# Kernel optimization log

Hardware: AMD Instinct MI355X
Metric: run time of the kernel (lower is better)

## Reference

```python
import jax, jax.numpy as jnp
import numpy as np

N_SURF, N_GRAPH, K_EIG = 30000, 12000, 128
C_IN_SURF, C_IN_GRAPH, C_OUT = 5, 20, 1
HID = 64  # C_width // 2
N_BLOCK = 4
NEIGH_TH = 8.0
BOX = 90.0
E_GRAPH = 192000


def _build_bipartite(rng):
    # exact math of compute_bipartite_graphs: cdist < neigh_th, w = exp(-d/sigma)
    verts = rng.random((N_SURF, 3), dtype=np.float32) * BOX
    pos = rng.random((N_GRAPH, 3), dtype=np.float32) * BOX
    sigma = NEIGH_TH / 2.0
    srcs, dsts, ws = [], [], []
    pn = (pos * pos).sum(-1)
    for s in range(0, N_SURF, 2048):
        ch = verts[s:s + 2048]
        d2 = (ch * ch).sum(-1)[:, None] + pn[None, :] - 2.0 * ch @ pos.T
        d = np.sqrt(np.maximum(d2, 0.0))
        ii, jj = np.where(d < NEIGH_TH)
        srcs.append(ii + s)
        dsts.append(jj + N_SURF)  # graph nodes offset by n_surf
        ws.append(np.exp(-d[ii, jj] / sigma))
    return (np.concatenate(srcs).astype(np.int64),
            np.concatenate(dsts).astype(np.int64),
            np.concatenate(ws).astype(np.float32))


def setup_inputs() -> dict:
    key = jax.random.key(0)
    ks = iter(jax.random.split(key, 64))
    rng = np.random.default_rng(0)
    bi_surf, bi_graph, bi_w = _build_bipartite(rng)

    def rn(shape, scale=0.05):
        return jax.random.normal(next(ks), shape, jnp.float32) * scale

    inp = {
        'x_surf': rn((N_SURF, C_IN_SURF), 1.0),
        'x_graph': rn((N_GRAPH, C_IN_GRAPH), 1.0),
        'mass': jax.random.uniform(next(ks), (N_SURF,), jnp.float32) + 0.1,
        'evals': jnp.sort(jax.random.uniform(next(ks), (K_EIG,), jnp.float32)) * 100.0,
        'evecs': rn((N_SURF, K_EIG), 1.0) / np.sqrt(N_SURF),
        'bi_w': jnp.asarray(bi_w),
        'lin1_w': rn((C_IN_SURF, HID)), 'lin1_b': jnp.zeros((HID,), jnp.float32),
        'lin2_w': rn((C_IN_GRAPH, HID)), 'lin2_b': jnp.zeros((HID,), jnp.float32),
        'diff_time': jax.random.uniform(next(ks), (N_BLOCK, HID), jnp.float32) * 0.1 + 1e-3,
        'mlp_w0': rn((N_BLOCK, 2 * HID, HID)), 'mlp_b0': jnp.zeros((N_BLOCK, HID), jnp.float32),
        'mlp_w1': rn((N_BLOCK, HID, HID)), 'mlp_b1': jnp.zeros((N_BLOCK, HID), jnp.float32),
        'mlp_w2': rn((N_BLOCK, HID, HID)), 'mlp_b2': jnp.zeros((N_BLOCK, HID), jnp.float32),
        'gcn_w1': rn((N_BLOCK, HID, HID)), 'gcn_b1': jnp.zeros((N_BLOCK, HID), jnp.float32),
        'gcn_w2': rn((N_BLOCK, HID, HID)), 'gcn_b2': jnp.zeros((N_BLOCK, HID), jnp.float32),
        'gs_w': rn((N_BLOCK - 1, HID, HID)), 'gs_b': jnp.zeros((N_BLOCK - 1, HID), jnp.float32),
        'gs_w_last': rn((HID, C_OUT)), 'gs_b_last': jnp.zeros((C_OUT,), jnp.float32),
        'sg_w': rn((N_BLOCK - 1, HID, HID)), 'sg_b': jnp.zeros((N_BLOCK - 1, HID), jnp.float32),
        'sg_w_last': rn((HID, C_OUT)), 'sg_b_last': jnp.zeros((C_OUT,), jnp.float32),
        'graph_edge_index': jax.random.randint(next(ks), (2, E_GRAPH), 0, N_GRAPH, jnp.int64),
        'bi_surf': jnp.asarray(bi_surf),
        'bi_graph': jnp.asarray(bi_graph),
    }
    return inp


def gcn_conv(x, W, b, src, dst, ew, n):
    # PyG GCNConv: sym-normalized aggregation with self loops (weight 1)
    h = x @ W
    w = ew if ew is not None else jnp.ones(src.shape, x.dtype)
    deg = jnp.ones((n,), x.dtype).at[dst].add(w)
    dinv = jnp.where(deg > 0, jax.lax.rsqrt(deg), 0.0)
    norm = dinv[src] * dinv[dst] * w
    out = jnp.zeros((n, h.shape[1]), x.dtype).at[dst].add(norm[:, None] * h[src])
    return out + (dinv * dinv)[:, None] * h + b


def reference(x_surf, x_graph, mass, evals, evecs, bi_w,
              lin1_w, lin1_b, lin2_w, lin2_b,
              diff_time, mlp_w0, mlp_b0, mlp_w1, mlp_b1, mlp_w2, mlp_b2,
              gcn_w1, gcn_b1, gcn_w2, gcn_b2,
              gs_w, gs_b, gs_w_last, gs_b_last,
              sg_w, sg_b, sg_w_last, sg_b_last,
              graph_edge_index, bi_surf, bi_graph):
    n_surf, n_graph = x_surf.shape[0], x_graph.shape[0]
    n_tot = n_surf + n_graph
    diff_x = x_surf @ lin1_w + lin1_b            # [Ns, HID]
    g_x = x_graph @ lin2_w + lin2_b              # [Ng, HID]
    gsrc, gdst = graph_edge_index[0], graph_edge_index[1]

    for i in range(N_BLOCK):
        # --- DiffusionNet block (spectral diffusion + MLP + skip) ---
        t = jnp.clip(diff_time[i], 1e-8)
        x_spec = evecs.T @ (mass[:, None] * diff_x)                  # [K, HID]
        x_diffuse = evecs @ (jnp.exp(-evals[:, None] * t[None, :]) * x_spec)
        feat = jnp.concatenate([diff_x, x_diffuse], axis=-1)
        h = jax.nn.relu(feat @ mlp_w0[i] + mlp_b0[i])
        h = jax.nn.relu(h @ mlp_w1[i] + mlp_b1[i])
        h = h @ mlp_w2[i] + mlp_b2[i]
        diff_x = diff_x + h
        # --- internal GCN on molecular graph (use_distance=False) ---
        hg = jax.nn.relu(gcn_conv(g_x, gcn_w1[i], gcn_b1[i], gsrc, gdst, None, n_graph))
        g_x = gcn_conv(hg, gcn_w2[i], gcn_b2[i], gsrc, gdst, None, n_graph)
        # --- bipartite mixing over combined node set ---
        x_cat = jnp.concatenate([diff_x, g_x], axis=0)               # [Ns+Ng, HID]
        if i < N_BLOCK - 1:
            new_surf = gcn_conv(x_cat, gs_w[i], gs_b[i], bi_graph, bi_surf, bi_w, n_tot)[:n_surf]
            new_graph = gcn_conv(x_cat, sg_w[i], sg_b[i], bi_surf, bi_graph, bi_w, n_tot)[n_surf:]
        else:
            new_surf = gcn_conv(x_cat, gs_w_last, gs_b_last, bi_graph, bi_surf, bi_w, n_tot)[:n_surf]
            new_graph = gcn_conv(x_cat, sg_w_last, sg_b_last, bi_surf, bi_graph, bi_w, n_tot)[n_surf:]
        diff_x, g_x = new_surf, new_graph

    return jnp.concatenate([diff_x, g_x], axis=0)  # [Ns+Ng, C_out]
```

## Files before the change

### kernel.cpp

```cpp
#include <hip/hip_runtime.h>

#define N_SURF 30000
#define N_GRAPH 12000
#define K_EIG 128
#define HID 64
#define E_GRAPH 192000
#define NPART 240

static inline int cdiv(int a, int b) { return (a + b - 1) / b; }

__global__ void k_fill(float* __restrict__ p, float v, int n) {
    int t = blockIdx.x * blockDim.x + threadIdx.x;
    if (t < n) p[t] = v;
}

__global__ void k_filli(int* __restrict__ p, int v, int n) {
    int t = blockIdx.x * blockDim.x + threadIdx.x;
    if (t < n) p[t] = v;
}

__global__ void k_to_dinv(float* __restrict__ p, int n) {
    int t = blockIdx.x * blockDim.x + threadIdx.x;
    if (t < n) p[t] = 1.0f / sqrtf(p[t]);
}

__global__ void k_deg_hist_bi(const int* __restrict__ bs, const int* __restrict__ bg,
                              const float* __restrict__ w, float* __restrict__ deg_s,
                              float* __restrict__ deg_g, int* __restrict__ cnt_s,
                              int* __restrict__ cnt_g, int E) {
    int t = blockIdx.x * blockDim.x + threadIdx.x;
    if (t < E) {
        int s = bs[t], g = bg[t] - N_SURF;
        float wv = w[t];
        atomicAdd(&deg_s[s], wv);
        atomicAdd(&deg_g[g], wv);
        atomicAdd(&cnt_s[s], 1);
        atomicAdd(&cnt_g[g], 1);
    }
}

__global__ void k_deg_hist_gr(const int* __restrict__ gdst, float* __restrict__ deg,
                              int* __restrict__ cnt, int E) {
    int t = blockIdx.x * blockDim.x + threadIdx.x;
    if (t < E) {
        int d = gdst[t];
        atomicAdd(&deg[d], 1.0f);
        atomicAdd(&cnt[d], 1);
    }
}

__global__ __launch_bounds__(256) void k_scan(const int* __restrict__ cnt,
                                              int* __restrict__ rowptr, int n) {
    __shared__ int part[256];
    int per = (n + 255) / 256;
    int lo = threadIdx.x * per, hi = min(lo + per, n);
    int s = 0;
    for (int i = lo; i < hi; ++i) s += cnt[i];
    part[threadIdx.x] = s;
    __syncthreads();
    for (int off = 1; off < 256; off <<= 1) {
        int v = (threadIdx.x >= off) ? part[threadIdx.x - off] : 0;
        __syncthreads();
        part[threadIdx.x] += v;
        __syncthreads();
    }
    int base = (threadIdx.x == 0) ? 0 : part[threadIdx.x - 1];
    for (int i = lo; i < hi; ++i) { rowptr[i] = base; base += cnt[i]; }
    if (threadIdx.x == 0) rowptr[n] = part[255];
}

__global__ void k_fill_csr_s_seq(const int* __restrict__ bs, const int* __restrict__ bg,
                                 const float* __restrict__ w, const float* __restrict__ dinv_s,
                                 int2* __restrict__ csr, int E) {
    int t = blockIdx.x * blockDim.x + threadIdx.x;
    if (t >= E) return;
    int s = bs[t], g = bg[t] - N_SURF;
    csr[t] = make_int2(g, __float_as_int(dinv_s[s] * w[t]));
}

__global__ void k_fill_csr_g(const int* __restrict__ bs, const int* __restrict__ bg,
                             const float* __restrict__ w, const float* __restrict__ dinv_g,
                             const int* __restrict__ rp, int* __restrict__ cur,
                             int2* __restrict__ csr, int E) {
    int t = blockIdx.x * blockDim.x + threadIdx.x;
    if (t >= E) return;
    int s = bs[t], g = bg[t] - N_SURF;
    int pp = rp[g] + atomicAdd(&cur[g], 1);
    csr[pp] = make_int2(s, __float_as_int(dinv_g[g] * w[t]));
}

__global__ void k_fill_csr_gr(const int* __restrict__ ei, const float* __restrict__ dinv,
                              const int* __restrict__ rp, int* __restrict__ cur,
                              int2* __restrict__ csr, int E) {
    int t = blockIdx.x * blockDim.x + threadIdx.x;
    if (t >= E) return;
    int s = ei[t], d = ei[E + t];
    int pp = rp[d] + atomicAdd(&cur[d], 1);
    csr[pp] = make_int2(s, __float_as_int(dinv[s] * dinv[d]));
}

__global__ void k_lin(const float* __restrict__ X, const float* __restrict__ W,
                      const float* __restrict__ b, float* __restrict__ out, int M, int K) {
    int t = blockIdx.x * blockDim.x + threadIdx.x;
    if (t >= M * HID) return;
    int r = t >> 6, h = t & 63;
    float acc = b[h];
    for (int k = 0; k < K; ++k) acc = fmaf(X[r * K + k], W[k * HID + h], acc);
    out[t] = acc;
}

__global__ __launch_bounds__(256) void k_spec_part(const float* __restrict__ evecs,
                                                   const float* __restrict__ mass,
                                                   const float* __restrict__ dx,
                                                   float* __restrict__ partial) {
    __shared__ float evs[32 * 128];
    __shared__ float xms[32 * 64];
    const int h = threadIdx.x & 63, eg = threadIdx.x >> 6;
    float acc[32];
#pragma unroll
    for (int i = 0; i < 32; ++i) acc[i] = 0.f;
    for (int r0 = blockIdx.x * 32; r0 < N_SURF; r0 += gridDim.x * 32) {
        __syncthreads();
        for (int idx = threadIdx.x; idx < 32 * 128; idx += 256) {
            int rr = idx >> 7, k = idx & 127;
            int row = r0 + rr;
            evs[idx] = (row < N_SURF) ? evecs[(size_t)row * 128 + k] : 0.f;
        }
        for (int idx = threadIdx.x; idx < 32 * 64; idx += 256) {
            int rr = idx >> 6, c = idx & 63;
            int row = r0 + rr;
            xms[idx] = (row < N_SURF) ? mass[row] * dx[(size_t)row * 64 + c] : 0.f;
        }
        __syncthreads();
        for (int rr = 0; rr < 32; ++rr) {
            float xv = xms[rr * 64 + h];
            const float* ep = &evs[rr * 128 + eg * 32];
#pragma unroll
            for (int e = 0; e < 32; ++e) acc[e] = fmaf(ep[e], xv, acc[e]);
        }
    }
    float* outp = &partial[(size_t)blockIdx.x * 8192];
#pragma unroll
    for (int e = 0; e < 32; ++e) outp[(eg * 32 + e) * 64 + h] = acc[e];
}

__global__ void k_spec_reduce_bscale(const float* __restrict__ partial,
                                     const float* __restrict__ evals,
                                     const float* __restrict__ t,
                                     float* __restrict__ Bsc) {
    int idx = blockIdx.x * blockDim.x + threadIdx.x;
    if (idx >= 128 * 64) return;
    int k = idx >> 6, h = idx & 63;
    float s = 0.f;
    for (int b = 0; b < NPART; ++b) s += partial[(size_t)b * 8192 + idx];
    float tt = fmaxf(t[h], 1e-8f);
    Bsc[idx] = expf(-evals[k] * tt) * s;
}

template <int K, bool RELU_A>
__global__ __launch_bounds__(256) void k_gemm64(const float* __restrict__ A1,
                                                const float* __restrict__ A2, int M1,
                                                const float* __restrict__ B,
                                                float* __restrict__ C, int M) {
    __shared__ float Bs[K * 64];
    __shared__ float As[64 * K];
    for (int idx = threadIdx.x; idx < K * 64; idx += 256) Bs[idx] = B[idx];
    const int h = threadIdx.x & 63, rg = threadIdx.x >> 6;
    for (int r0 = blockIdx.x * 64; r0 < M; r0 += gridDim.x * 64) {
        __syncthreads();
        for (int idx = threadIdx.x; idx < 64 * K; idx += 256) {
            int rr = idx / K, k = idx - rr * K;
            int row = r0 + rr;
            float v = 0.f;
            if (row < M) {
                v = (row < M1) ? A1[(size_t)row * K + k]
                               : A2[(size_t)(row - M1) * K + k];
                if (RELU_A) v = fmaxf(v, 0.f);
            }
            As[idx] = v;
        }
        __syncthreads();
        float acc[16];
#pragma unroll
        for (int i = 0; i < 16; ++i) acc[i] = 0.f;
        for (int k = 0; k < K; k += 4) {
            float b0 = Bs[(k + 0) * 64 + h], b1 = Bs[(k + 1) * 64 + h];
            float b2 = Bs[(k + 2) * 64 + h], b3 = Bs[(k + 3) * 64 + h];
#pragma unroll
            for (int i = 0; i < 16; ++i) {
                const float* ap = &As[(rg * 16 + i) * K + k];
                acc[i] = fmaf(ap[0], b0, fmaf(ap[1], b1, fmaf(ap[2], b2, fmaf(ap[3], b3, acc[i]))));
            }
        }
#pragma unroll
        for (int i = 0; i < 16; ++i) {
            int row = r0 + rg * 16 + i;
            if (row < M) C[(size_t)row * 64 + h] = acc[i];
        }
    }
}

__global__ __launch_bounds__(256) void k_gemm128_r32(const float* __restrict__ A,
                                                     const float* __restrict__ B,
                                                     float* __restrict__ C, int M) {
    __shared__ float Bs[128 * 64];
    __shared__ float As[32 * 128];
    for (int idx = threadIdx.x; idx < 128 * 64; idx += 256) Bs[idx] = B[idx];
    const int h = threadIdx.x & 63, rg = threadIdx.x >> 6;
    for (int r0 = blockIdx.x * 32; r0 < M; r0 += gridDim.x * 32) {
        __syncthreads();
        for (int idx = threadIdx.x; idx < 32 * 128; idx += 256) {
            int rr = idx >> 7, k = idx & 127;
            int row = r0 + rr;
            As[idx] = (row < M) ? A[(size_t)row * 128 + k] : 0.f;
        }
        __syncthreads();
        float acc[8];
#pragma unroll
        for (int i = 0; i < 8; ++i) acc[i] = 0.f;
        for (int k = 0; k < 128; k += 4) {
            float b0 = Bs[(k + 0) * 64 + h], b1 = Bs[(k + 1) * 64 + h];
            float b2 = Bs[(k + 2) * 64 + h], b3 = Bs[(k + 3) * 64 + h];
#pragma unroll
            for (int i = 0; i < 8; ++i) {
                const float* ap = &As[(rg * 8 + i) * 128 + k];
                acc[i] = fmaf(ap[0], b0, fmaf(ap[1], b1, fmaf(ap[2], b2, fmaf(ap[3], b3, acc[i]))));
            }
        }
#pragma unroll
        for (int i = 0; i < 8; ++i) {
            int row = r0 + rg * 8 + i;
            if (row < M) C[(size_t)row * 64 + h] = acc[i];
        }
    }
}

__global__ __launch_bounds__(256) void k_mlp(float* __restrict__ dx, const float* __restrict__ xd,
                                             const float* __restrict__ w0, const float* __restrict__ b0,
                                             const float* __restrict__ w1, const float* __restrict__ b1,
                                             const float* __restrict__ w2, const float* __restrict__ b2,
                                             int M) {
    __shared__ float w0s[128 * 64];
    __shared__ float w1s[64 * 64];
    __shared__ float w2s[64 * 64];
    __shared__ float bsh[3][64];
    __shared__ float feat[4][128];
    __shared__ float h1s[4][64];
    __shared__ float h2s[4][64];
    for (int idx = threadIdx.x; idx < 8192; idx += 256) w0s[idx] = w0[idx];
    for (int idx = threadIdx.x; idx < 4096; idx += 256) { w1s[idx] = w1[idx]; w2s[idx] = w2[idx]; }
    if (threadIdx.x < 64) {
        bsh[0][threadIdx.x] = b0[threadIdx.x];
        bsh[1][threadIdx.x] = b1[threadIdx.x];
        bsh[2][threadIdx.x] = b2[threadIdx.x];
    }
    const int h = threadIdx.x & 63, rg = threadIdx.x >> 6;
    for (int r0 = blockIdx.x * 4; r0 < M; r0 += gridDim.x * 4) {
        int r = r0 + rg;
        __syncthreads();
        feat[rg][h] = dx[(size_t)r * 64 + h];
        feat[rg][64 + h] = xd[(size_t)r * 64 + h];
        __syncthreads();
        float acc = bsh[0][h];
        for (int k = 0; k < 128; k += 4) {
            const float* fp = &feat[rg][k];
            acc = fmaf(fp[0], w0s[(k + 0) * 64 + h],
                  fmaf(fp[1], w0s[(k + 1) * 64 + h],
                  fmaf(fp[2], w0s[(k + 2) * 64 + h],
                  fmaf(fp[3], w0s[(k + 3) * 64 + h], acc))));
        }
        h1s[rg][h] = fmaxf(acc, 0.f);
        __syncthreads();
        acc = bsh[1][h];
        for (int k = 0; k < 64; k += 4) {
            const float* fp = &h1s[rg][k];
            acc = fmaf(fp[0], w1s[(k + 0) * 64 + h],
                  fmaf(fp[1], w1s[(k + 1) * 64 + h],
                  fmaf(fp[2], w1s[(k + 2) * 64 + h],
                  fmaf(fp[3], w1s[(k + 3) * 64 + h], acc))));
        }
        h2s[rg][h] = fmaxf(acc, 0.f);
        __syncthreads();
        acc = bsh[2][h];
        for (int k = 0; k < 64; k += 4) {
            const float* fp = &h2s[rg][k];
            acc = fmaf(fp[0], w2s[(k + 0) * 64 + h],
                  fmaf(fp[1], w2s[(k + 1) * 64 + h],
                  fmaf(fp[2], w2s[(k + 2) * 64 + h],
                  fmaf(fp[3], w2s[(k + 3) * 64 + h], acc))));
        }
        dx[(size_t)r * 64 + h] += acc;
    }
}

__global__ __launch_bounds__(256) void k_gather64(
    const int* __restrict__ rowptr, const int2* __restrict__ csr,
    const float* __restrict__ Hsrc, const float* __restrict__ Hself,
    const float* __restrict__ dinv, const float* __restrict__ b,
    float* __restrict__ out, int M) {
    int r = blockIdx.x * 4 + (threadIdx.x >> 6);
    int h = threadIdx.x & 63;
    if (r >= M) return;
    int e0 = rowptr[r], e1 = rowptr[r + 1];
    float dv = dinv[r];
    float acc = fmaf(dv * dv, Hself[(size_t)r * 64 + h], b[h]);
    int e = e0;
    for (; e + 1 < e1; e += 2) {
        int2 c0 = csr[e], c1 = csr[e + 1];
        acc = fmaf(__int_as_float(c0.y), Hsrc[(size_t)c0.x * 64 + h], acc);
        acc = fmaf(__int_as_float(c1.y), Hsrc[(size_t)c1.x * 64 + h], acc);
    }
    if (e < e1) {
        int2 c = csr[e];
        acc = fmaf(__int_as_float(c.y), Hsrc[(size_t)c.x * 64 + h], acc);
    }
    out[(size_t)r * 64 + h] = acc;
}

__global__ __launch_bounds__(256) void k_gather1(
    const int* __restrict__ rowptr, const int2* __restrict__ csr,
    const float* __restrict__ H1src, const float* __restrict__ H1self,
    const float* __restrict__ dinv, const float* __restrict__ b,
    float* __restrict__ out, int M) {
    int r = blockIdx.x * 4 + (threadIdx.x >> 6);
    int l = threadIdx.x & 63;
    if (r >= M) return;
    int e0 = rowptr[r], e1 = rowptr[r + 1];
    float acc = 0.f;
    for (int e = e0 + l; e < e1; e += 64) {
        int2 c = csr[e];
        acc = fmaf(__int_as_float(c.y), H1src[c.x], acc);
    }
    for (int off = 32; off; off >>= 1) acc += __shfl_down(acc, off, 64);
    if (l == 0) {
        float dv = dinv[r];
        out[r] = fmaf(dv * dv, H1self[r], b[0]) + acc;
    }
}

__global__ void k_gemv64c(const float* __restrict__ A1, const float* __restrict__ A2, int M1,
                          const float* __restrict__ w, float* __restrict__ out, int M) {
    int gid = blockIdx.x * blockDim.x + threadIdx.x;
    int r = gid >> 6, l = gid & 63;
    if (r >= M) return;
    const float* row = (r < M1) ? &A1[(size_t)r * 64] : &A2[(size_t)(r - M1) * 64];
    float v = row[l] * w[l];
    for (int off = 32; off; off >>= 1) v += __shfl_down(v, off, 64);
    if (l == 0) out[r] = v;
}

extern "C" void kernel_launch(void* const* d_in, const int* in_sizes, int n_in,
                              void* d_out, int out_size, void* d_ws, size_t ws_size,
                              hipStream_t stream) {
    const float* x_surf   = (const float*)d_in[0];
    const float* x_graph  = (const float*)d_in[1];
    const float* mass     = (const float*)d_in[2];
    const float* evals    = (const float*)d_in[3];
    const float* evecs    = (const float*)d_in[4];
    const float* bi_w     = (const float*)d_in[5];
    const float* lin1_w   = (const float*)d_in[6];
    const float* lin1_b   = (const float*)d_in[7];
    const float* lin2_w   = (const float*)d_in[8];
    const float* lin2_b   = (const float*)d_in[9];
    const float* diff_time= (const float*)d_in[10];
    const float* mlp_w0   = (const float*)d_in[11];
    const float* mlp_b0   = (const float*)d_in[12];
    const float* mlp_w1   = (const float*)d_in[13];
    const float* mlp_b1   = (const float*)d_in[14];
    const float* mlp_w2   = (const float*)d_in[15];
    const float* mlp_b2   = (const float*)d_in[16];
    const float* gcn_w1   = (const float*)d_in[17];
    const float* gcn_b1   = (const float*)d_in[18];
    const float* gcn_w2   = (const float*)d_in[19];
    const float* gcn_b2   = (const float*)d_in[20];
    const float* gs_w     = (const float*)d_in[21];
    const float* gs_b     = (const float*)d_in[22];
    const float* gs_w_last= (const float*)d_in[23];
    const float* gs_b_last= (const float*)d_in[24];
    const float* sg_w     = (const float*)d_in[25];
    const float* sg_b     = (const float*)d_in[26];
    const float* sg_w_last= (const float*)d_in[27];
    const float* sg_b_last= (const float*)d_in[28];
    const int* graph_ei   = (const int*)d_in[29];
    const int* bi_s       = (const int*)d_in[30];
    const int* bi_g       = (const int*)d_in[31];
    const int E = in_sizes[5];
    float* out = (float*)d_out;

    float* p = (float*)d_ws;
    float* surfA = p; p += (size_t)N_SURF * 64;
    float* surfB = p; p += (size_t)N_SURF * 64;
    float* xd    = p; p += (size_t)N_SURF * 64;
    float* hcat  = p; p += (size_t)(N_SURF + N_GRAPH) * 64;
    float* gA    = p; p += (size_t)N_GRAPH * 64;
    float* gB    = p; p += (size_t)N_GRAPH * 64;
    float* tmpg  = p; p += (size_t)N_GRAPH * 64;
    float* hg    = p; p += (size_t)N_GRAPH * 64;
    float* partial = p; p += (size_t)NPART * 8192;
    float* Bsc   = p; p += 128 * 64;
    float* dinv_s  = p; p += N_SURF;
    float* dinv_g  = p; p += N_GRAPH;
    float* dinv_gr = p; p += N_GRAPH;
    int* cnt_s = (int*)p; p += N_SURF;
    int* cnt_g = (int*)p; p += N_GRAPH;
    int* cnt_gr= (int*)p; p += N_GRAPH;
    int* rp_s  = (int*)p; p += N_SURF + 1;
    int* rp_g  = (int*)p; p += N_GRAPH + 1;
    int* rp_gr = (int*)p; p += N_GRAPH + 1;
    p += ((size_t)p & 4) ? 1 : 0;
    int2* csr_s  = (int2*)p; p += 2 * (size_t)E;
    int2* csr_g  = (int2*)p; p += 2 * (size_t)E;
    int2* csr_gr = (int2*)p; p += 2 * (size_t)E_GRAPH;

    float* hg_part = hcat + (size_t)N_SURF * 64;
    float* dx  = surfA;
    float* nsx = surfB;
    float* gx  = gA;
    float* gx2 = gB;

    k_lin<<<cdiv(N_SURF * 64, 256), 256, 0, stream>>>(x_surf, lin1_w, lin1_b, dx, N_SURF, 5);
    k_lin<<<cdiv(N_GRAPH * 64, 256), 256, 0, stream>>>(x_graph, lin2_w, lin2_b, gx, N_GRAPH, 20);
    k_fill<<<cdiv(N_SURF, 256), 256, 0, stream>>>(dinv_s, 1.f, N_SURF);
    k_fill<<<cdiv(N_GRAPH, 256), 256, 0, stream>>>(dinv_g, 1.f, N_GRAPH);
    k_fill<<<cdiv(N_GRAPH, 256), 256, 0, stream>>>(dinv_gr, 1.f, N_GRAPH);
    k_filli<<<cdiv(N_SURF, 256), 256, 0, stream>>>(cnt_s, 0, N_SURF);
    k_filli<<<cdiv(N_GRAPH, 256), 256, 0, stream>>>(cnt_g, 0, N_GRAPH);
    k_filli<<<cdiv(N_GRAPH, 256), 256, 0, stream>>>(cnt_gr, 0, N_GRAPH);
    k_deg_hist_bi<<<cdiv(E, 256), 256, 0, stream>>>(bi_s, bi_g, bi_w, dinv_s, dinv_g,
                                                    cnt_s, cnt_g, E);
    k_deg_hist_gr<<<cdiv(E_GRAPH, 256), 256, 0, stream>>>(graph_ei + E_GRAPH, dinv_gr, cnt_gr, E_GRAPH);
    k_to_dinv<<<cdiv(N_SURF, 256), 256, 0, stream>>>(dinv_s, N_SURF);
    k_to_dinv<<<cdiv(N_GRAPH, 256), 256, 0, stream>>>(dinv_g, N_GRAPH);
    k_to_dinv<<<cdiv(N_GRAPH, 256), 256, 0, stream>>>(dinv_gr, N_GRAPH);
    k_scan<<<1, 256, 0, stream>>>(cnt_s, rp_s, N_SURF);
    k_scan<<<1, 256, 0, stream>>>(cnt_g, rp_g, N_GRAPH);
    k_scan<<<1, 256, 0, stream>>>(cnt_gr, rp_gr, N_GRAPH);
    k_fill_csr_s_seq<<<cdiv(E, 256), 256, 0, stream>>>(bi_s, bi_g, bi_w, dinv_s, csr_s, E);
    k_filli<<<cdiv(N_GRAPH, 256), 256, 0, stream>>>(cnt_g, 0, N_GRAPH);
    k_filli<<<cdiv(N_GRAPH, 256), 256, 0, stream>>>(cnt_gr, 0, N_GRAPH);
    k_fill_csr_g<<<cdiv(E, 256), 256, 0, stream>>>(bi_s, bi_g, bi_w, dinv_g, rp_g, cnt_g, csr_g, E);
    k_fill_csr_gr<<<cdiv(E_GRAPH, 256), 256, 0, stream>>>(graph_ei, dinv_gr, rp_gr, cnt_gr,
                                                          csr_gr, E_GRAPH);

    const int gG = cdiv(N_GRAPH, 64);
    const int gC = cdiv(N_SURF + N_GRAPH, 64);

    for (int i = 0; i < 4; ++i) {
        k_spec_part<<<NPART, 256, 0, stream>>>(evecs, mass, dx, partial);
        k_spec_reduce_bscale<<<32, 256, 0, stream>>>(partial, evals, diff_time + i * 64, Bsc);
        k_gemm128_r32<<<938, 256, 0, stream>>>(evecs, Bsc, xd, N_SURF);
        k_mlp<<<938, 256, 0, stream>>>(dx, xd, mlp_w0 + i * 8192, mlp_b0 + i * 64,
                                       mlp_w1 + i * 4096, mlp_b1 + i * 64,
                                       mlp_w2 + i * 4096, mlp_b2 + i * 64, N_SURF);
        k_gemm64<64, false><<<gG, 256, 0, stream>>>(gx, gx, N_GRAPH, gcn_w1 + i * 4096, hg, N_GRAPH);
        k_gather64<<<cdiv(N_GRAPH, 4), 256, 0, stream>>>(rp_gr, csr_gr, hg, hg, dinv_gr,
                                                         gcn_b1 + i * 64, tmpg, N_GRAPH);
        k_gemm64<64, true><<<gG, 256, 0, stream>>>(tmpg, tmpg, N_GRAPH, gcn_w2 + i * 4096, hg, N_GRAPH);
        k_gather64<<<cdiv(N_GRAPH, 4), 256, 0, stream>>>(rp_gr, csr_gr, hg, hg, dinv_gr,
                                                         gcn_b2 + i * 64, gx2, N_GRAPH);

        if (i < 3) {
            k_gemm64<64, false><<<gC, 256, 0, stream>>>(dx, gx2, N_SURF, gs_w + i * 4096,
                                                        hcat, N_SURF + N_GRAPH);
            k_gather64<<<cdiv(N_SURF, 4), 256, 0, stream>>>(rp_s, csr_s, hg_part, hcat, dinv_s,
                                                            gs_b + i * 64, nsx, N_SURF);
            k_gemm64<64, false><<<gC, 256, 0, stream>>>(dx, gx2, N_SURF, sg_w + i * 4096,
                                                        hcat, N_SURF + N_GRAPH);
            k_gather64<<<cdiv(N_GRAPH, 4), 256, 0, stream>>>(rp_g, csr_g, hcat, hg_part, dinv_g,
                                                             sg_b + i * 64, gx, N_GRAPH);
            float* t = dx; dx = nsx; nsx = t;
        } else {
            float* h1 = hcat;
            float* h1g = hcat + N_SURF;
            k_gemv64c<<<cdiv((N_SURF + N_GRAPH) * 64, 256), 256, 0, stream>>>(
                dx, gx2, N_SURF, gs_w_last, h1, N_SURF + N_GRAPH);
            k_gather1<<<cdiv(N_SURF, 4), 256, 0, stream>>>(rp_s, csr_s, h1g, h1, dinv_s,
                                                           gs_b_last, out, N_SURF);
            k_gemv64c<<<cdiv((N_SURF + N_GRAPH) * 64, 256), 256, 0, stream>>>(
                dx, gx2, N_SURF, sg_w_last, h1, N_SURF + N_GRAPH);
            k_gather1<<<cdiv(N_GRAPH, 4), 256, 0, stream>>>(rp_g, csr_g, h1, h1g, dinv_g,
                                                            sg_b_last, out + N_SURF, N_GRAPH);
        }
    }
}
```

Baseline: 1.827 ms.

## Fuse dual bipartite GEMMs and gathers; rebuild degree setup with sorted segments and shared histograms

```diff
diff --git a/kernel.cpp b/kernel.cpp
--- a/kernel.cpp
+++ b/kernel.cpp
@@ -19,33 +19,65 @@
     if (t < n) p[t] = v;
 }
 
-__global__ void k_to_dinv(float* __restrict__ p, int n) {
-    int t = blockIdx.x * blockDim.x + threadIdx.x;
-    if (t < n) p[t] = 1.0f / sqrtf(p[t]);
-}
-
-__global__ void k_deg_hist_bi(const int* __restrict__ bs, const int* __restrict__ bg,
-                              const float* __restrict__ w, float* __restrict__ deg_s,
-                              float* __restrict__ deg_g, int* __restrict__ cnt_s,
-                              int* __restrict__ cnt_g, int E) {
-    int t = blockIdx.x * blockDim.x + threadIdx.x;
-    if (t < E) {
-        int s = bs[t], g = bg[t] - N_SURF;
-        float wv = w[t];
-        atomicAdd(&deg_s[s], wv);
-        atomicAdd(&deg_g[g], wv);
-        atomicAdd(&cnt_s[s], 1);
-        atomicAdd(&cnt_g[g], 1);
-    }
-}
-
-__global__ void k_deg_hist_gr(const int* __restrict__ gdst, float* __restrict__ deg,
-                              int* __restrict__ cnt, int E) {
-    int t = blockIdx.x * blockDim.x + threadIdx.x;
-    if (t < E) {
-        int d = gdst[t];
-        atomicAdd(&deg[d], 1.0f);
-        atomicAdd(&cnt[d], 1);
+__global__ void k_rp_sorted(const int* __restrict__ bs, int* __restrict__ rp, int E) {
+    int t = blockIdx.x * blockDim.x + threadIdx.x;
+    if (t >= E) return;
+    if (t == 0) {
+        int b0 = bs[0];
+        for (int s = 0; s <= b0; ++s) rp[s] = 0;
+        int bl = bs[E - 1];
+        for (int s = bl + 1; s <= N_SURF; ++s) rp[s] = E;
+    } else {
+        int a = bs[t - 1], b = bs[t];
+        for (int s = a + 1; s <= b; ++s) rp[s] = t;
+    }
+}
+
+__global__ void k_dinv_s_seg(const int* __restrict__ rp, const float* __restrict__ w,
+                             float* __restrict__ dinv_s, int M) {
+    int r = blockIdx.x * blockDim.x + threadIdx.x;
+    if (r >= M) return;
+    int e0 = rp[r], e1 = rp[r + 1];
+    float s = 1.0f;
+    for (int e = e0; e < e1; ++e) s += w[e];
+    dinv_s[r] = rsqrtf(s);
+}
+
+__global__ __launch_bounds__(256) void k_hist_cnt_g(const int* __restrict__ idx, int off,
+                                                    int* __restrict__ cnt, int E) {
+    __shared__ int hc[N_GRAPH];
+    for (int i = threadIdx.x; i < N_GRAPH; i += 256) hc[i] = 0;
+    __syncthreads();
+    for (int t = blockIdx.x * 256 + threadIdx.x; t < E; t += gridDim.x * 256)
+        atomicAdd(&hc[idx[t] - off], 1);
+    __syncthreads();
+    for (int i = threadIdx.x; i < N_GRAPH; i += 256) {
+        int v = hc[i];
+        if (v) atomicAdd(&cnt[i], v);
+    }
+}
+
+__global__ __launch_bounds__(256) void k_hist_w_g(const int* __restrict__ bg,
+                                                  const float* __restrict__ w,
+                                                  float* __restrict__ deg, int E) {
+    __shared__ float hw[N_GRAPH];
+    for (int i = threadIdx.x; i < N_GRAPH; i += 256) hw[i] = 0.f;
+    __syncthreads();
+    for (int t = blockIdx.x * 256 + threadIdx.x; t < E; t += gridDim.x * 256)
+        atomicAdd(&hw[bg[t] - N_SURF], w[t]);
+    __syncthreads();
+    for (int i = threadIdx.x; i < N_GRAPH; i += 256) {
+        float v = hw[i];
+        if (v != 0.f) atomicAdd(&deg[i], v);
+    }
+}
+
+__global__ void k_dinv_g_both(const float* __restrict__ deg_w, const int* __restrict__ cnt_gr,
+                              float* __restrict__ dinv_g, float* __restrict__ dinv_gr, int n) {
+    int t = blockIdx.x * blockDim.x + threadIdx.x;
+    if (t < n) {
+        dinv_g[t] = rsqrtf(1.0f + deg_w[t]);
+        dinv_gr[t] = rsqrtf(1.0f + (float)cnt_gr[t]);
     }
 }
 
@@ -74,8 +106,7 @@
                                  int2* __restrict__ csr, int E) {
     int t = blockIdx.x * blockDim.x + threadIdx.x;
     if (t >= E) return;
-    int s = bs[t], g = bg[t] - N_SURF;
-    csr[t] = make_int2(g, __float_as_int(dinv_s[s] * w[t]));
+    csr[t] = make_int2(bg[t] - N_SURF, __float_as_int(dinv_s[bs[t]] * w[t]));
 }
 
 __global__ void k_fill_csr_g(const int* __restrict__ bs, const int* __restrict__ bg,
@@ -157,24 +188,24 @@
     Bsc[idx] = expf(-evals[k] * tt) * s;
 }
 
-template <int K, bool RELU_A>
+template <bool RELU_A>
 __global__ __launch_bounds__(256) void k_gemm64(const float* __restrict__ A1,
                                                 const float* __restrict__ A2, int M1,
                                                 const float* __restrict__ B,
                                                 float* __restrict__ C, int M) {
-    __shared__ float Bs[K * 64];
-    __shared__ float As[64 * K];
-    for (int idx = threadIdx.x; idx < K * 64; idx += 256) Bs[idx] = B[idx];
+    __shared__ float Bs[64 * 64];
+    __shared__ float As[64 * 64];
+    for (int idx = threadIdx.x; idx < 64 * 64; idx += 256) Bs[idx] = B[idx];
     const int h = threadIdx.x & 63, rg = threadIdx.x >> 6;
     for (int r0 = blockIdx.x * 64; r0 < M; r0 += gridDim.x * 64) {
         __syncthreads();
-        for (int idx = threadIdx.x; idx < 64 * K; idx += 256) {
-            int rr = idx / K, k = idx - rr * K;
+        for (int idx = threadIdx.x; idx < 64 * 64; idx += 256) {
+            int rr = idx >> 6, k = idx & 63;
             int row = r0 + rr;
             float v = 0.f;
             if (row < M) {
-                v = (row < M1) ? A1[(size_t)row * K + k]
-                               : A2[(size_t)(row - M1) * K + k];
+                v = (row < M1) ? A1[(size_t)row * 64 + k]
+                               : A2[(size_t)(row - M1) * 64 + k];
                 if (RELU_A) v = fmaxf(v, 0.f);
             }
             As[idx] = v;
@@ -183,12 +214,12 @@
         float acc[16];
 #pragma unroll
         for (int i = 0; i < 16; ++i) acc[i] = 0.f;
-        for (int k = 0; k < K; k += 4) {
+        for (int k = 0; k < 64; k += 4) {
             float b0 = Bs[(k + 0) * 64 + h], b1 = Bs[(k + 1) * 64 + h];
             float b2 = Bs[(k + 2) * 64 + h], b3 = Bs[(k + 3) * 64 + h];
 #pragma unroll
             for (int i = 0; i < 16; ++i) {
-                const float* ap = &As[(rg * 16 + i) * K + k];
+                const float* ap = &As[(rg * 16 + i) * 64 + k];
                 acc[i] = fmaf(ap[0], b0, fmaf(ap[1], b1, fmaf(ap[2], b2, fmaf(ap[3], b3, acc[i]))));
             }
         }
@@ -196,6 +227,54 @@
         for (int i = 0; i < 16; ++i) {
             int row = r0 + rg * 16 + i;
             if (row < M) C[(size_t)row * 64 + h] = acc[i];
+        }
+    }
+}
+
+__global__ __launch_bounds__(256) void k_gemm64_dual(const float* __restrict__ A1,
+                                                     const float* __restrict__ A2, int M1,
+                                                     const float* __restrict__ Ba,
+                                                     const float* __restrict__ Bb,
+                                                     float* __restrict__ Ca,
+                                                     float* __restrict__ Cb, int M) {
+    __shared__ float Bsa[64 * 64];
+    __shared__ float Bsb[64 * 64];
+    __shared__ float As[64 * 64];
+    for (int idx = threadIdx.x; idx < 64 * 64; idx += 256) { Bsa[idx] = Ba[idx]; Bsb[idx] = Bb[idx]; }
+    const int h = threadIdx.x & 63, rg = threadIdx.x >> 6;
+    for (int r0 = blockIdx.x * 64; r0 < M; r0 += gridDim.x * 64) {
+        __syncthreads();
+        for (int idx = threadIdx.x; idx < 64 * 64; idx += 256) {
+            int rr = idx >> 6, k = idx & 63;
+            int row = r0 + rr;
+            float v = 0.f;
+            if (row < M) {
+                v = (row < M1) ? A1[(size_t)row * 64 + k]
+                               : A2[(size_t)(row - M1) * 64 + k];
+            }
+            As[idx] = v;
+        }
+        __syncthreads();
+        float acca[16], accb[16];
+#pragma unroll
+        for (int i = 0; i < 16; ++i) { acca[i] = 0.f; accb[i] = 0.f; }
+        for (int k = 0; k < 64; k += 2) {
+            float a0 = Bsa[(k + 0) * 64 + h], a1 = Bsa[(k + 1) * 64 + h];
+            float b0 = Bsb[(k + 0) * 64 + h], b1 = Bsb[(k + 1) * 64 + h];
+#pragma unroll
+            for (int i = 0; i < 16; ++i) {
+                const float* ap = &As[(rg * 16 + i) * 64 + k];
+                acca[i] = fmaf(ap[0], a0, fmaf(ap[1], a1, acca[i]));
+                accb[i] = fmaf(ap[0], b0, fmaf(ap[1], b1, accb[i]));
+            }
+        }
+#pragma unroll
+        for (int i = 0; i < 16; ++i) {
+            int row = r0 + rg * 16 + i;
+            if (row < M) {
+                Ca[(size_t)row * 64 + h] = acca[i];
+                Cb[(size_t)row * 64 + h] = accb[i];
+            }
         }
     }
 }
@@ -317,36 +396,88 @@
     out[(size_t)r * 64 + h] = acc;
 }
 
-__global__ __launch_bounds__(256) void k_gather1(
-    const int* __restrict__ rowptr, const int2* __restrict__ csr,
-    const float* __restrict__ H1src, const float* __restrict__ H1self,
-    const float* __restrict__ dinv, const float* __restrict__ b,
-    float* __restrict__ out, int M) {
-    int r = blockIdx.x * 4 + (threadIdx.x >> 6);
-    int l = threadIdx.x & 63;
-    if (r >= M) return;
-    int e0 = rowptr[r], e1 = rowptr[r + 1];
-    float acc = 0.f;
-    for (int e = e0 + l; e < e1; e += 64) {
-        int2 c = csr[e];
-        acc = fmaf(__int_as_float(c.y), H1src[c.x], acc);
-    }
-    for (int off = 32; off; off >>= 1) acc += __shfl_down(acc, off, 64);
-    if (l == 0) {
-        float dv = dinv[r];
-        out[r] = fmaf(dv * dv, H1self[r], b[0]) + acc;
-    }
-}
-
-__global__ void k_gemv64c(const float* __restrict__ A1, const float* __restrict__ A2, int M1,
-                          const float* __restrict__ w, float* __restrict__ out, int M) {
+__global__ __launch_bounds__(256) void k_gather_bi(
+    const int* __restrict__ rp_s, const int2* __restrict__ csr_s, const float* __restrict__ hcatA,
+    const int* __restrict__ rp_g, const int2* __restrict__ csr_g, const float* __restrict__ hcatB,
+    const float* __restrict__ dinv_s, const float* __restrict__ dinv_g,
+    const float* __restrict__ b_gs, const float* __restrict__ b_sg,
+    float* __restrict__ out_surf, float* __restrict__ out_graph) {
+    int rr = blockIdx.x * 4 + (threadIdx.x >> 6);
+    int h = threadIdx.x & 63;
+    if (rr < N_SURF) {
+        int e0 = rp_s[rr], e1 = rp_s[rr + 1];
+        float dv = dinv_s[rr];
+        const float* src = hcatA + (size_t)N_SURF * 64;
+        float acc = fmaf(dv * dv, hcatA[(size_t)rr * 64 + h], b_gs[h]);
+        for (int e = e0; e < e1; ++e) {
+            int2 c = csr_s[e];
+            acc = fmaf(__int_as_float(c.y), src[(size_t)c.x * 64 + h], acc);
+        }
+        out_surf[(size_t)rr * 64 + h] = acc;
+    } else if (rr < N_SURF + N_GRAPH) {
+        int r = rr - N_SURF;
+        int e0 = rp_g[r], e1 = rp_g[r + 1];
+        float dv = dinv_g[r];
+        float acc = fmaf(dv * dv, hcatB[(size_t)rr * 64 + h], b_sg[h]);
+        for (int e = e0; e < e1; ++e) {
+            int2 c = csr_g[e];
+            acc = fmaf(__int_as_float(c.y), hcatB[(size_t)c.x * 64 + h], acc);
+        }
+        out_graph[(size_t)r * 64 + h] = acc;
+    }
+}
+
+__global__ void k_gemv_dual(const float* __restrict__ A1, const float* __restrict__ A2, int M1,
+                            const float* __restrict__ wA, const float* __restrict__ wB,
+                            float* __restrict__ oA, float* __restrict__ oB, int M) {
     int gid = blockIdx.x * blockDim.x + threadIdx.x;
     int r = gid >> 6, l = gid & 63;
     if (r >= M) return;
     const float* row = (r < M1) ? &A1[(size_t)r * 64] : &A2[(size_t)(r - M1) * 64];
-    float v = row[l] * w[l];
-    for (int off = 32; off; off >>= 1) v += __shfl_down(v, off, 64);
-    if (l == 0) out[r] = v;
+    float v = row[l];
+    float va = v * wA[l], vb = v * wB[l];
+    for (int off = 32; off; off >>= 1) {
+        va += __shfl_down(va, off, 64);
+        vb += __shfl_down(vb, off, 64);
+    }
+    if (l == 0) { oA[r] = va; oB[r] = vb; }
+}
+
+__global__ __launch_bounds__(256) void k_gather1_bi(
+    const int* __restrict__ rp_s, const int2* __restrict__ csr_s, const float* __restrict__ h1A,
+    const int* __restrict__ rp_g, const int2* __restrict__ csr_g, const float* __restrict__ h1B,
+    const float* __restrict__ dinv_s, const float* __restrict__ dinv_g,
+    const float* __restrict__ b_gs, const float* __restrict__ b_sg,
+    float* __restrict__ out) {
+    int rr = blockIdx.x * 4 + (threadIdx.x >> 6);
+    int l = threadIdx.x & 63;
+    if (rr < N_SURF) {
+        int e0 = rp_s[rr], e1 = rp_s[rr + 1];
+        const float* src = h1A + N_SURF;
+        float acc = 0.f;
+        for (int e = e0 + l; e < e1; e += 64) {
+            int2 c = csr_s[e];
+            acc = fmaf(__int_as_float(c.y), src[c.x], acc);
+        }
+        for (int off = 32; off; off >>= 1) acc += __shfl_down(acc, off, 64);
+        if (l == 0) {
+            float dv = dinv_s[rr];
+            out[rr] = fmaf(dv * dv, h1A[rr], b_gs[0]) + acc;
+        }
+    } else if (rr < N_SURF + N_GRAPH) {
+        int r = rr - N_SURF;
+        int e0 = rp_g[r], e1 = rp_g[r + 1];
+        float acc = 0.f;
+        for (int e = e0 + l; e < e1; e += 64) {
+            int2 c = csr_g[e];
+            acc = fmaf(__int_as_float(c.y), h1B[c.x], acc);
+        }
+        for (int off = 32; off; off >>= 1) acc += __shfl_down(acc, off, 64);
+        if (l == 0) {
+            float dv = dinv_g[r];
+            out[rr] = fmaf(dv * dv, h1B[rr], b_sg[0]) + acc;
+        }
+    }
 }
 
 extern "C" void kernel_launch(void* const* d_in, const int* in_sizes, int n_in,
@@ -391,7 +522,8 @@
     float* surfA = p; p += (size_t)N_SURF * 64;
     float* surfB = p; p += (size_t)N_SURF * 64;
     float* xd    = p; p += (size_t)N_SURF * 64;
-    float* hcat  = p; p += (size_t)(N_SURF + N_GRAPH) * 64;
+    float* hcatA = p; p += (size_t)(N_SURF + N_GRAPH) * 64;
+    float* hcatB = p; p += (size_t)(N_SURF + N_GRAPH) * 64;
     float* gA    = p; p += (size_t)N_GRAPH * 64;
     float* gB    = p; p += (size_t)N_GRAPH * 64;
     float* tmpg  = p; p += (size_t)N_GRAPH * 64;
@@ -401,7 +533,7 @@
     float* dinv_s  = p; p += N_SURF;
     float* dinv_g  = p; p += N_GRAPH;
     float* dinv_gr = p; p += N_GRAPH;
-    int* cnt_s = (int*)p; p += N_SURF;
+    float* deg_gw  = p; p += N_GRAPH;
     int* cnt_g = (int*)p; p += N_GRAPH;
     int* cnt_gr= (int*)p; p += N_GRAPH;
     int* rp_s  = (int*)p; p += N_SURF + 1;
@@ -412,7 +544,6 @@
     int2* csr_g  = (int2*)p; p += 2 * (size_t)E;
     int2* csr_gr = (int2*)p; p += 2 * (size_t)E_GRAPH;
 
-    float* hg_part = hcat + (size_t)N_SURF * 64;
     float* dx  = surfA;
     float* nsx = surfB;
     float* gx  = gA;
@@ -420,21 +551,17 @@
 
     k_lin<<<cdiv(N_SURF * 64, 256), 256, 0, stream>>>(x_surf, lin1_w, lin1_b, dx, N_SURF, 5);
     k_lin<<<cdiv(N_GRAPH * 64, 256), 256, 0, stream>>>(x_graph, lin2_w, lin2_b, gx, N_GRAPH, 20);
-    k_fill<<<cdiv(N_SURF, 256), 256, 0, stream>>>(dinv_s, 1.f, N_SURF);
-    k_fill<<<cdiv(N_GRAPH, 256), 256, 0, stream>>>(dinv_g, 1.f, N_GRAPH);
-    k_fill<<<cdiv(N_GRAPH, 256), 256, 0, stream>>>(dinv_gr, 1.f, N_GRAPH);
-    k_filli<<<cdiv(N_SURF, 256), 256, 0, stream>>>(cnt_s, 0, N_SURF);
+    k_rp_sorted<<<cdiv(E, 256), 256, 0, stream>>>(bi_s, rp_s, E);
+    k_dinv_s_seg<<<cdiv(N_SURF, 256), 256, 0, stream>>>(rp_s, bi_w, dinv_s, N_SURF);
     k_filli<<<cdiv(N_GRAPH, 256), 256, 0, stream>>>(cnt_g, 0, N_GRAPH);
     k_filli<<<cdiv(N_GRAPH, 256), 256, 0, stream>>>(cnt_gr, 0, N_GRAPH);
-    k_deg_hist_bi<<<cdiv(E, 256), 256, 0, stream>>>(bi_s, bi_g, bi_w, dinv_s, dinv_g,
-                                                    cnt_s, cnt_g, E);
-    k_deg_hist_gr<<<cdiv(E_GRAPH, 256), 256, 0, stream>>>(graph_ei + E_GRAPH, dinv_gr, cnt_gr, E_GRAPH);
-    k_to_dinv<<<cdiv(N_SURF, 256), 256, 0, stream>>>(dinv_s, N_SURF);
-    k_to_dinv<<<cdiv(N_GRAPH, 256), 256, 0, stream>>>(dinv_g, N_GRAPH);
-    k_to_dinv<<<cdiv(N_GRAPH, 256), 256, 0, stream>>>(dinv_gr, N_GRAPH);
-    k_scan<<<1, 256, 0, stream>>>(cnt_s, rp_s, N_SURF);
+    k_fill<<<cdiv(N_GRAPH, 256), 256, 0, stream>>>(deg_gw, 0.f, N_GRAPH);
+    k_hist_cnt_g<<<32, 256, 0, stream>>>(bi_g, N_SURF, cnt_g, E);
+    k_hist_w_g<<<32, 256, 0, stream>>>(bi_g, bi_w, deg_gw, E);
+    k_hist_cnt_g<<<32, 256, 0, stream>>>(graph_ei + E_GRAPH, 0, cnt_gr, E_GRAPH);
     k_scan<<<1, 256, 0, stream>>>(cnt_g, rp_g, N_GRAPH);
     k_scan<<<1, 256, 0, stream>>>(cnt_gr, rp_gr, N_GRAPH);
+    k_dinv_g_both<<<cdiv(N_GRAPH, 256), 256, 0, stream>>>(deg_gw, cnt_gr, dinv_g, dinv_gr, N_GRAPH);
     k_fill_csr_s_seq<<<cdiv(E, 256), 256, 0, stream>>>(bi_s, bi_g, bi_w, dinv_s, csr_s, E);
     k_filli<<<cdiv(N_GRAPH, 256), 256, 0, stream>>>(cnt_g, 0, N_GRAPH);
     k_filli<<<cdiv(N_GRAPH, 256), 256, 0, stream>>>(cnt_gr, 0, N_GRAPH);
@@ -452,34 +579,29 @@
         k_mlp<<<938, 256, 0, stream>>>(dx, xd, mlp_w0 + i * 8192, mlp_b0 + i * 64,
                                        mlp_w1 + i * 4096, mlp_b1 + i * 64,
                                        mlp_w2 + i * 4096, mlp_b2 + i * 64, N_SURF);
-        k_gemm64<64, false><<<gG, 256, 0, stream>>>(gx, gx, N_GRAPH, gcn_w1 + i * 4096, hg, N_GRAPH);
+        k_gemm64<false><<<gG, 256, 0, stream>>>(gx, gx, N_GRAPH, gcn_w1 + i * 4096, hg, N_GRAPH);
         k_gather64<<<cdiv(N_GRAPH, 4), 256, 0, stream>>>(rp_gr, csr_gr, hg, hg, dinv_gr,
                                                          gcn_b1 + i * 64, tmpg, N_GRAPH);
-        k_gemm64<64, true><<<gG, 256, 0, stream>>>(tmpg, tmpg, N_GRAPH, gcn_w2 + i * 4096, hg, N_GRAPH);
+        k_gemm64<true><<<gG, 256, 0, stream>>>(tmpg, tmpg, N_GRAPH, gcn_w2 + i * 4096, hg, N_GRAPH);
         k_gather64<<<cdiv(N_GRAPH, 4), 256, 0, stream>>>(rp_gr, csr_gr, hg, hg, dinv_gr,
                                                          gcn_b2 + i * 64, gx2, N_GRAPH);
 
         if (i < 3) {
-            k_gemm64<64, false><<<gC, 256, 0, stream>>>(dx, gx2, N_SURF, gs_w + i * 4096,
-                                                        hcat, N_SURF + N_GRAPH);
-            k_gather64<<<cdiv(N_SURF, 4), 256, 0, stream>>>(rp_s, csr_s, hg_part, hcat, dinv_s,
-                                                            gs_b + i * 64, nsx, N_SURF);
-            k_gemm64<64, false><<<gC, 256, 0, stream>>>(dx, gx2, N_SURF, sg_w + i * 4096,
-                                                        hcat, N_SURF + N_GRAPH);
-            k_gather64<<<cdiv(N_GRAPH, 4), 256, 0, stream>>>(rp_g, csr_g, hcat, hg_part, dinv_g,
-                                                             sg_b + i * 64, gx, N_GRAPH);
+            k_gemm64_dual<<<gC, 256, 0, stream>>>(dx, gx2, N_SURF, gs_w + i * 4096,
+                                                  sg_w + i * 4096, hcatA, hcatB,
+                                                  N_SURF + N_GRAPH);
+            k_gather_bi<<<cdiv(N_SURF + N_GRAPH, 4), 256, 0, stream>>>(
+                rp_s, csr_s, hcatA, rp_g, csr_g, hcatB, dinv_s, dinv_g,
+                gs_b + i * 64, sg_b + i * 64, nsx, gx);
             float* t = dx; dx = nsx; nsx = t;
         } else {
-            float* h1 = hcat;
-            float* h1g = hcat + N_SURF;
-            k_gemv64c<<<cdiv((N_SURF + N_GRAPH) * 64, 256), 256, 0, stream>>>(
-                dx, gx2, N_SURF, gs_w_last, h1, N_SURF + N_GRAPH);
-            k_gather1<<<cdiv(N_SURF, 4), 256, 0, stream>>>(rp_s, csr_s, h1g, h1, dinv_s,
-                                                           gs_b_last, out, N_SURF);
-            k_gemv64c<<<cdiv((N_SURF + N_GRAPH) * 64, 256), 256, 0, stream>>>(
-                dx, gx2, N_SURF, sg_w_last, h1, N_SURF + N_GRAPH);
-            k_gather1<<<cdiv(N_GRAPH, 4), 256, 0, stream>>>(rp_g, csr_g, h1, h1g, dinv_g,
-                                                            sg_b_last, out + N_SURF, N_GRAPH);
-        }
-    }
-}
+            float* h1A = hcatA;
+            float* h1B = hcatB;
+            k_gemv_dual<<<cdiv((N_SURF + N_GRAPH) * 64, 256), 256, 0, stream>>>(
+                dx, gx2, N_SURF, gs_w_last, sg_w_last, h1A, h1B, N_SURF + N_GRAPH);
+            k_gather1_bi<<<cdiv(N_SURF + N_GRAPH, 4), 256, 0, stream>>>(
+                rp_s, csr_s, h1A, rp_g, csr_g, h1B, dinv_s, dinv_g,
+                gs_b_last, sg_b_last, out);
+        }
+    }
+}
```

Result: faster. 1.724 ms (-5.6%).
